# Kernel optimization log

Hardware: AMD Instinct MI355X
Metric: run time of the kernel (lower is better)

The kernel has to match this reference:

```python
import jax, jax.numpy as jnp
import numpy as np

N_A, N_P = 100000, 150000
N = N_A + N_P          # total nodes in concatenated feature matrix
D = 128                # emb_dim == hidden
C = 16                 # num_classes
E = 2000000            # nnz per relation


def setup_inputs() -> dict:
    key = jax.random.key(0)
    ks = jax.random.split(key, 16)
    s = 1.0 / np.sqrt(D)
    # coefficients as in init_coe: uniform(-b, b) then L1-normalized, coe_num = 1+2+2 = 5
    bound = np.sqrt(3.0 / 5)
    coe_np = np.random.RandomState(0).uniform(-bound, bound, 5)
    coe_np = coe_np / np.sum(np.abs(coe_np))
    return {
        "x0": jax.random.normal(ks[0], (N_A, D), jnp.float32),
        "x1": jax.random.normal(ks[1], (N_P, D), jnp.float32),
        "vals_ap": jax.random.uniform(ks[2], (E,), jnp.float32) * 0.01,
        "vals_pa": jax.random.uniform(ks[3], (E,), jnp.float32) * 0.01,
        # AP: rows are A nodes [0, N_A), cols are P nodes [N_A, N)
        "rows_ap": jax.random.randint(ks[4], (E,), 0, N_A, jnp.int32),
        "cols_ap": jax.random.randint(ks[5], (E,), N_A, N, jnp.int32),
        # PA: rows are P nodes [N_A, N), cols are A nodes [0, N_A)
        "rows_pa": jax.random.randint(ks[6], (E,), N_A, N, jnp.int32),
        "cols_pa": jax.random.randint(ks[7], (E,), 0, N_A, jnp.int32),
        "Wp0": jax.random.normal(ks[8], (D, D), jnp.float32) * s,
        "Wp1": jax.random.normal(ks[9], (D, D), jnp.float32) * s,
        "W1": jax.random.normal(ks[10], (D, D), jnp.float32) * s,
        "b1": jnp.zeros((D,), jnp.float32),
        "W2": jax.random.normal(ks[11], (D, C), jnp.float32) * s,
        "b2": jnp.zeros((C,), jnp.float32),
        "coe": jnp.asarray(coe_np, jnp.float32),
    }


def _spmm(rows, cols, vals, h):
    # sparse [N,N] @ dense [N,D] via gather + segment-sum
    return jax.ops.segment_sum(vals[:, None] * h[cols], rows, num_segments=N)


def _normalize(x):
    mean = x.mean(axis=1, keepdims=True)
    std = jnp.std(x, axis=1, keepdims=True, ddof=1)  # torch std is unbiased
    z = (x - mean) / std
    return jnp.where(jnp.isnan(z), 0.0, z)


def _power_pass(x, coe, ap, pa, first_order):
    # first_order: tuple of relation names in hop-1 order ("AP","PA") or ("PA","AP")
    rel = {"AP": ap, "PA": pa}
    res = coe[0] * x
    h = {}
    for ci, r in enumerate(first_order):
        h[r] = _spmm(*rel[r], x)
        res = res + coe[1 + ci] * h[r]
    # hop 2: compose relation j[:2] with previous result j[2:]
    second = [r + first_order[1 - i] for i, r in enumerate(first_order)]
    for ci, j in enumerate(second):
        out = _spmm(*rel[j[:2]], h[j[2:]])
        res = res + coe[3 + ci] * out
    return res


def reference(x0, x1, vals_ap, vals_pa, rows_ap, cols_ap, rows_pa, cols_pa,
              Wp0, Wp1, W1, b1, W2, b2, coe):
    ap = (rows_ap, cols_ap, vals_ap)
    pa = (rows_pa, cols_pa, vals_pa)
    # per-type projection then concat along node axis
    x = jnp.concatenate([x0 @ Wp0, x1 @ Wp1], axis=0)  # [N, D]
    x = jax.nn.relu(x @ W1 + b1)
    x = _normalize(x)
    # pass 1: lis = {1: [AP, PA], 2: [APPA, PAAP]}
    x = _power_pass(x, coe, ap, pa, ("AP", "PA"))
    # pass 2 (transposed series): lis_t = {1: [PA, AP], 2: [PAAP, APPA]}
    res = _power_pass(x, coe, ap, pa, ("PA", "AP"))
    return res @ W2 + b2  # [N, C]
```

## Files before the change

### kernel.cpp

```cpp
#include <hip/hip_runtime.h>
#include <hip/hip_bf16.h>


typedef float f32x2 __attribute__((ext_vector_type(2)));
typedef float f32x4 __attribute__((ext_vector_type(4)));

__device__ inline unsigned short f2bf(float x) {
    unsigned b = __float_as_uint(x);
    unsigned r = (b + 0x7fffu + ((b >> 16) & 1u)) >> 16;
    return (unsigned short)r;
}
__device__ inline float bflo(unsigned u) { return __uint_as_float(u << 16); }
__device__ inline float bfhi(unsigned u) { return __uint_as_float(u & 0xffff0000u); }

__device__ inline unsigned pk_fp8x4(float a, float b, float c, float d) {
    int v = __builtin_amdgcn_cvt_pk_fp8_f32(a, b, 0, false);
    v = __builtin_amdgcn_cvt_pk_fp8_f32(c, d, v, true);
    return (unsigned)v;
}

__global__ __launch_bounds__(128) void fuse_w(const float* __restrict__ Wp0,
                                              const float* __restrict__ Wp1,
                                              const float* __restrict__ W1,
                                              float* __restrict__ M0,
                                              float* __restrict__ M1) {
    int m = blockIdx.x >> 7;
    int i = blockIdx.x & 127;
    const float* Wp = m ? Wp1 : Wp0;
    float* M = m ? M1 : M0;
    __shared__ float r[128];
    int t = threadIdx.x;
    r[t] = Wp[i * 128 + t];
    __syncthreads();
    float acc = 0.f;
    #pragma unroll 8
    for (int k = 0; k < 128; ++k) acc += r[k] * W1[k * 128 + t];
    M[i * 128 + t] = acc;
}

__global__ __launch_bounds__(256) void gemm_relu_norm(const float* __restrict__ xin,
                                                      const float* __restrict__ M,
                                                      const float* __restrict__ b1,
                                                      unsigned short* __restrict__ xbf,
                                                      unsigned char* __restrict__ x8,
                                                      int nrows) {
    __shared__ float Wl[64 * 128];
    __shared__ float xs[32 * 128];
    int t = threadIdx.x;
    long row0 = (long)blockIdx.x * 32;
    int rows_this = nrows - (int)row0;
    if (rows_this > 32) rows_this = 32;

    #pragma unroll
    for (int it = 0; it < 4; ++it) {
        int g4 = it * 256 + t;
        int g = g4 * 4;
        int rl = g >> 7, c = g & 127;
        float4 val = {0.f, 0.f, 0.f, 0.f};
        if (rl < rows_this) val = *(const float4*)(xin + (row0 + rl) * 128 + c);
        *(float4*)&xs[rl * 128 + c] = val;
    }

    int r0 = (t >> 5) * 4;
    int c0 = (t & 31) * 4;
    float acc[4][4];
    #pragma unroll
    for (int i = 0; i < 4; ++i)
        #pragma unroll
        for (int j = 0; j < 4; ++j) acc[i][j] = 0.f;

    for (int h = 0; h < 2; ++h) {
        __syncthreads();
        #pragma unroll
        for (int it = 0; it < 8; ++it) {
            int g4 = it * 256 + t;
            ((float4*)Wl)[g4] = ((const float4*)(M + h * 8192))[g4];
        }
        __syncthreads();
        #pragma unroll 4
        for (int k = 0; k < 64; ++k) {
            float4 w = *(float4*)&Wl[k * 128 + c0];
            int kk = h * 64 + k;
            #pragma unroll
            for (int i = 0; i < 4; ++i) {
                float a = xs[(r0 + i) * 128 + kk];
                acc[i][0] += a * w.x;
                acc[i][1] += a * w.y;
                acc[i][2] += a * w.z;
                acc[i][3] += a * w.w;
            }
        }
    }

    float4 bb = *(const float4*)(b1 + c0);
    #pragma unroll
    for (int i = 0; i < 4; ++i) {
        float o0 = acc[i][0] + bb.x; o0 = o0 > 0.f ? o0 : 0.f;
        float o1 = acc[i][1] + bb.y; o1 = o1 > 0.f ? o1 : 0.f;
        float o2 = acc[i][2] + bb.z; o2 = o2 > 0.f ? o2 : 0.f;
        float o3 = acc[i][3] + bb.w; o3 = o3 > 0.f ? o3 : 0.f;
        float s = o0 + o1 + o2 + o3;
        #pragma unroll
        for (int m = 16; m >= 1; m >>= 1) s += __shfl_xor(s, m);
        float mean = s * (1.0f / 128.0f);
        float d0 = o0 - mean, d1 = o1 - mean, d2 = o2 - mean, d3 = o3 - mean;
        float q = d0 * d0 + d1 * d1 + d2 * d2 + d3 * d3;
        #pragma unroll
        for (int m = 16; m >= 1; m >>= 1) q += __shfl_xor(q, m);
        float inv = 0.f;
        if (q > 0.f) inv = 1.0f / sqrtf(q * (1.0f / 127.0f));
        int row = r0 + i;
        if (row < rows_this) {
            float z0 = d0 * inv, z1 = d1 * inv, z2 = d2 * inv, z3 = d3 * inv;
            uint2 pk;
            pk.x = (unsigned)f2bf(z0) | ((unsigned)f2bf(z1) << 16);
            pk.y = (unsigned)f2bf(z2) | ((unsigned)f2bf(z3) << 16);
            *(uint2*)(xbf + (row0 + row) * 128 + c0) = pk;
            *(unsigned*)(x8 + (row0 + row) * 128 + c0) = pk_fp8x4(z0, z1, z2, z3);
        }
    }
}

__global__ __launch_bounds__(256) void count_rows(const int* __restrict__ rows, int E,
                                                  int* __restrict__ cnt) {
    int i = (blockIdx.x * 256 + threadIdx.x) * 4;
    if (i + 4 <= E) {
        int4 r = *(const int4*)(rows + i);
        atomicAdd(&cnt[r.x], 1);
        atomicAdd(&cnt[r.y], 1);
        atomicAdd(&cnt[r.z], 1);
        atomicAdd(&cnt[r.w], 1);
    } else {
        for (; i < E; ++i) atomicAdd(&cnt[rows[i]], 1);
    }
}

__global__ __launch_bounds__(256) void scan1(const int* __restrict__ cnt, int R,
                                             int* __restrict__ rp, int* __restrict__ bt) {
    __shared__ int lds[256];
    int t = threadIdx.x, b = blockIdx.x;
    int base = b * 4096 + t * 16;
    int v[16];
    int s = 0;
    #pragma unroll
    for (int i = 0; i < 16; ++i) {
        int idx = base + i;
        int c = (idx < R) ? cnt[idx] : 0;
        v[i] = s;
        s += c;
    }
    lds[t] = s;
    __syncthreads();
    for (int off = 1; off < 256; off <<= 1) {
        int x = (t >= off) ? lds[t - off] : 0;
        __syncthreads();
        lds[t] += x;
        __syncthreads();
    }
    int excl = lds[t] - s;
    #pragma unroll
    for (int i = 0; i < 16; ++i) {
        int idx = base + i;
        if (idx < R) rp[idx] = excl + v[i];
    }
    if (t == 0) bt[b] = lds[255];
}

__global__ __launch_bounds__(64) void scan2(const int* __restrict__ bt, int B,
                                            int* __restrict__ bo, int* __restrict__ rp,
                                            int R, int E2) {
    int t = threadIdx.x;
    int v = (t < B) ? bt[t] : 0;
    int inc = v;
    #pragma unroll
    for (int off = 1; off < 64; off <<= 1) {
        int y = __shfl_up(inc, off);
        if (t >= off) inc += y;
    }
    if (t < B) bo[t] = inc - v;
    if (t == 0) rp[R] = E2;
}

__global__ __launch_bounds__(256) void scan3(int* __restrict__ rp, const int* __restrict__ bo,
                                             int R) {
    int i = blockIdx.x * 256 + threadIdx.x;
    if (i < R) rp[i] = rp[i] + bo[i >> 12];
}

__global__ __launch_bounds__(256) void binit(const int* __restrict__ rp, int NR,
                                             int nbuck, int* __restrict__ bcur) {
    int b = blockIdx.x * 256 + threadIdx.x;
    if (b < nbuck) {
        int r = b << 9;
        if (r > NR) r = NR;
        bcur[b] = rp[r];
    }
}

__global__ __launch_bounds__(256) void partition_edges(const int* __restrict__ rows,
                                                       const int* __restrict__ cols,
                                                       const float* __restrict__ vals,
                                                       int E, int nbuck,
                                                       int* __restrict__ bcur,
                                                       int2* __restrict__ tmp) {
    __shared__ int hist[512];
    __shared__ int gbase[512];
    __shared__ int cnt2[512];
    int t = threadIdx.x;
    for (int b = t; b < nbuck; b += 256) { hist[b] = 0; cnt2[b] = 0; }
    __syncthreads();
    long base = (long)blockIdx.x * 4096;
    #pragma unroll
    for (int k = 0; k < 16; ++k) {
        long i = base + k * 256 + t;
        if (i < E) atomicAdd(&hist[rows[i] >> 9], 1);
    }
    __syncthreads();
    for (int b = t; b < nbuck; b += 256) {
        int h = hist[b];
        gbase[b] = h ? atomicAdd(&bcur[b], h) : 0;
    }
    __syncthreads();
    #pragma unroll
    for (int k = 0; k < 16; ++k) {
        long i = base + k * 256 + t;
        if (i < E) {
            int rl = rows[i];
            int b = rl >> 9;
            int rank = atomicAdd(&cnt2[b], 1);
            int2 rec;
            rec.x = ((rl - (b << 9)) << 18) | cols[i];
            rec.y = __float_as_int(vals[i]);
            tmp[gbase[b] + rank] = rec;
        }
    }
}

__global__ __launch_bounds__(1024) void place_edges(const int* __restrict__ rp,
                                                    const int2* __restrict__ tmp,
                                                    int NR,
                                                    int2* __restrict__ scv) {
    __shared__ int hist[512];
    __shared__ int hoff[512];
    int b = blockIdx.x;
    int srow = b << 9;
    int erow = srow + 512;
    if (erow > NR) erow = NR;
    int start = rp[srow], endp = rp[erow];
    int t = threadIdx.x;
    if (t < 512) hist[t] = 0;
    __syncthreads();

    for (int i = start + t; i < endp; i += 1024)
        atomicAdd(&hist[tmp[i].x >> 18], 1);
    __syncthreads();

    if (t < 512) hoff[t] = hist[t];
    __syncthreads();
    for (int off = 1; off < 512; off <<= 1) {
        int v = 0;
        if (t < 512 && t >= off) v = hoff[t - off];
        __syncthreads();
        if (t < 512) hoff[t] += v;
        __syncthreads();
    }
    if (t < 512) hoff[t] = start + hoff[t] - hist[t];
    __syncthreads();

    int i = start + t;
    for (; i + 3 * 1024 < endp; i += 4 * 1024) {
        int2 a0 = tmp[i];
        int2 a1 = tmp[i + 1024];
        int2 a2 = tmp[i + 2048];
        int2 a3 = tmp[i + 3072];
        int p0 = atomicAdd(&hoff[a0.x >> 18], 1);
        int p1 = atomicAdd(&hoff[a1.x >> 18], 1);
        int p2 = atomicAdd(&hoff[a2.x >> 18], 1);
        int p3 = atomicAdd(&hoff[a3.x >> 18], 1);
        int2 o0; o0.x = a0.x & 0x3ffff; o0.y = a0.y;
        int2 o1; o1.x = a1.x & 0x3ffff; o1.y = a1.y;
        int2 o2; o2.x = a2.x & 0x3ffff; o2.y = a2.y;
        int2 o3; o3.x = a3.x & 0x3ffff; o3.y = a3.y;
        scv[p0] = o0;
        scv[p1] = o1;
        scv[p2] = o2;
        scv[p3] = o3;
    }
    for (; i < endp; i += 1024) {
        int2 rec = tmp[i];
        int p = atomicAdd(&hoff[rec.x >> 18], 1);
        int2 o;
        o.x = rec.x & 0x3ffff;
        o.y = rec.y;
        scv[p] = o;
    }
}

#define DEC_FMA(qq, vv) do {                                                        \
    f32x2 vp_ = {(vv), (vv)};                                                       \
    acc[0] = __builtin_elementwise_fma(vp_, __builtin_amdgcn_cvt_pk_f32_fp8((qq).x, false), acc[0]); \
    acc[1] = __builtin_elementwise_fma(vp_, __builtin_amdgcn_cvt_pk_f32_fp8((qq).x, true),  acc[1]); \
    acc[2] = __builtin_elementwise_fma(vp_, __builtin_amdgcn_cvt_pk_f32_fp8((qq).y, false), acc[2]); \
    acc[3] = __builtin_elementwise_fma(vp_, __builtin_amdgcn_cvt_pk_f32_fp8((qq).y, true),  acc[3]); \
} while (0)

__device__ inline void spmm_core8(const int* __restrict__ rp,
                                  const int2* __restrict__ scv,
                                  const unsigned char* __restrict__ g8,
                                  int row, int f, f32x2* acc) {
    int beg = rp[row], end = rp[row + 1];
    int j = beg;
    if ((j & 1) && j < end) {
        int2 r0 = scv[j];
        uint2 q0 = *(const uint2*)(g8 + ((long)r0.x << 7) + f);
        float v0 = __int_as_float(r0.y);
        DEC_FMA(q0, v0);
        ++j;
    }
    for (; j + 8 <= end; j += 8) {
        int4 s01 = *(const int4*)(scv + j);
        int4 s23 = *(const int4*)(scv + j + 2);
        int4 s45 = *(const int4*)(scv + j + 4);
        int4 s67 = *(const int4*)(scv + j + 6);
        uint2 q0 = *(const uint2*)(g8 + ((long)s01.x << 7) + f);
        uint2 q1 = *(const uint2*)(g8 + ((long)s01.z << 7) + f);
        uint2 q2 = *(const uint2*)(g8 + ((long)s23.x << 7) + f);
        uint2 q3 = *(const uint2*)(g8 + ((long)s23.z << 7) + f);
        uint2 q4 = *(const uint2*)(g8 + ((long)s45.x << 7) + f);
        uint2 q5 = *(const uint2*)(g8 + ((long)s45.z << 7) + f);
        uint2 q6 = *(const uint2*)(g8 + ((long)s67.x << 7) + f);
        uint2 q7 = *(const uint2*)(g8 + ((long)s67.z << 7) + f);
        DEC_FMA(q0, __int_as_float(s01.y));
        DEC_FMA(q1, __int_as_float(s01.w));
        DEC_FMA(q2, __int_as_float(s23.y));
        DEC_FMA(q3, __int_as_float(s23.w));
        DEC_FMA(q4, __int_as_float(s45.y));
        DEC_FMA(q5, __int_as_float(s45.w));
        DEC_FMA(q6, __int_as_float(s67.y));
        DEC_FMA(q7, __int_as_float(s67.w));
    }
    for (; j + 2 <= end; j += 2) {
        int4 s01 = *(const int4*)(scv + j);
        uint2 q0 = *(const uint2*)(g8 + ((long)s01.x << 7) + f);
        uint2 q1 = *(const uint2*)(g8 + ((long)s01.z << 7) + f);
        DEC_FMA(q0, __int_as_float(s01.y));
        DEC_FMA(q1, __int_as_float(s01.w));
    }
    if (j < end) {
        int2 r0 = scv[j];
        uint2 q0 = *(const uint2*)(g8 + ((long)r0.x << 7) + f);
        float v0 = __int_as_float(r0.y);
        DEC_FMA(q0, v0);
    }
}

__global__ __launch_bounds__(256) void spmm_plain(const int* __restrict__ rp,
                                                  const int2* __restrict__ scv,
                                                  const unsigned char* __restrict__ x8,
                                                  unsigned short* __restrict__ houtbf,
                                                  unsigned char* __restrict__ hout8,
                                                  int R) {
    int wave = blockIdx.x * 4 + (threadIdx.x >> 6);
    int lane = threadIdx.x & 63;
    int row = wave * 4 + (lane >> 4);
    if (row >= R) return;
    int f = (lane & 15) << 3;
    f32x2 acc[4];
    #pragma unroll
    for (int i = 0; i < 4; ++i) acc[i] = (f32x2){0.f, 0.f};
    spmm_core8(rp, scv, x8, row, f, acc);
    uint4 o;
    o.x = (unsigned)f2bf(acc[0].x) | ((unsigned)f2bf(acc[0].y) << 16);
    o.y = (unsigned)f2bf(acc[1].x) | ((unsigned)f2bf(acc[1].y) << 16);
    o.z = (unsigned)f2bf(acc[2].x) | ((unsigned)f2bf(acc[2].y) << 16);
    o.w = (unsigned)f2bf(acc[3].x) | ((unsigned)f2bf(acc[3].y) << 16);
    *(uint4*)(houtbf + ((long)row << 7) + f) = o;
    uint2 o8;
    o8.x = pk_fp8x4(acc[0].x, acc[0].y, acc[1].x, acc[1].y);
    o8.y = pk_fp8x4(acc[2].x, acc[2].y, acc[3].x, acc[3].y);
    *(uint2*)(hout8 + ((long)row << 7) + f) = o8;
}

__global__ __launch_bounds__(256) void spmm_update(const int* __restrict__ rp,
                                                   const int2* __restrict__ scv,
                                                   const unsigned char* __restrict__ h8,
                                                   const unsigned short* __restrict__ hbf,
                                                   unsigned short* __restrict__ Xbf,
                                                   unsigned char* __restrict__ X8,
                                                   const float* __restrict__ coe,
                                                   int ihA, int iaA, int ihP, int iaP,
                                                   int NA, int R) {
    int wave = blockIdx.x * 4 + (threadIdx.x >> 6);
    int lane = threadIdx.x & 63;
    int row = wave * 4 + (lane >> 4);
    if (row >= R) return;
    int f = (lane & 15) << 3;
    f32x2 acc[4];
    #pragma unroll
    for (int i = 0; i < 4; ++i) acc[i] = (f32x2){0.f, 0.f};
    spmm_core8(rp, scv, h8, row, f, acc);

    float c0 = coe[0];
    float ch = coe[row < NA ? ihA : ihP];
    float ca = coe[row < NA ? iaA : iaP];
    long o = ((long)row << 7) + f;
    uint4 xv = *(const uint4*)(Xbf + o);
    uint4 hs = *(const uint4*)(hbf + o);
    float r[8];
    r[0] = c0 * bflo(xv.x) + ch * bflo(hs.x) + ca * acc[0].x;
    r[1] = c0 * bfhi(xv.x) + ch * bfhi(hs.x) + ca * acc[0].y;
    r[2] = c0 * bflo(xv.y) + ch * bflo(hs.y) + ca * acc[1].x;
    r[3] = c0 * bfhi(xv.y) + ch * bfhi(hs.y) + ca * acc[1].y;
    r[4] = c0 * bflo(xv.z) + ch * bflo(hs.z) + ca * acc[2].x;
    r[5] = c0 * bfhi(xv.z) + ch * bfhi(hs.z) + ca * acc[2].y;
    r[6] = c0 * bflo(xv.w) + ch * bflo(hs.w) + ca * acc[3].x;
    r[7] = c0 * bfhi(xv.w) + ch * bfhi(hs.w) + ca * acc[3].y;
    uint4 ob;
    ob.x = (unsigned)f2bf(r[0]) | ((unsigned)f2bf(r[1]) << 16);
    ob.y = (unsigned)f2bf(r[2]) | ((unsigned)f2bf(r[3]) << 16);
    ob.z = (unsigned)f2bf(r[4]) | ((unsigned)f2bf(r[5]) << 16);
    ob.w = (unsigned)f2bf(r[6]) | ((unsigned)f2bf(r[7]) << 16);
    *(uint4*)(Xbf + o) = ob;
    uint2 o8;
    o8.x = pk_fp8x4(r[0], r[1], r[2], r[3]);
    o8.y = pk_fp8x4(r[4], r[5], r[6], r[7]);
    *(uint2*)(X8 + o) = o8;
}

__global__ __launch_bounds__(256) void spmm_update_out(const int* __restrict__ rp,
                                                       const int2* __restrict__ scv,
                                                       const unsigned char* __restrict__ h8,
                                                       const unsigned short* __restrict__ hbf,
                                                       const unsigned short* __restrict__ Xbf,
                                                       const float* __restrict__ coe,
                                                       const float* __restrict__ W2,
                                                       const float* __restrict__ b2,
                                                       float* __restrict__ out,
                                                       int ihA, int iaA, int ihP, int iaP,
                                                       int NA, int R) {
    __shared__ float xs[16 * 132];
    __shared__ float wT[16 * 132];
    __shared__ float bs[16];
    int t = threadIdx.x;
    #pragma unroll
    for (int i = 0; i < 8; ++i) {
        int idx = i * 256 + t;
        wT[(idx & 15) * 132 + (idx >> 4)] = W2[idx];
    }
    if (t < 16) bs[t] = b2[t];

    int lane = t & 63;
    int rl = (t >> 6) * 4 + (lane >> 4);
    int row = blockIdx.x * 16 + rl;
    int f = (lane & 15) << 3;
    if (row < R) {
        f32x2 acc[4];
        #pragma unroll
        for (int i = 0; i < 4; ++i) acc[i] = (f32x2){0.f, 0.f};
        spmm_core8(rp, scv, h8, row, f, acc);
        float c0 = coe[0];
        float ch = coe[row < NA ? ihA : ihP];
        float ca = coe[row < NA ? iaA : iaP];
        long o = ((long)row << 7) + f;
        uint4 xv = *(const uint4*)(Xbf + o);
        uint4 hs = *(const uint4*)(hbf + o);
        float* x = &xs[rl * 132 + f];
        x[0] = c0 * bflo(xv.x) + ch * bflo(hs.x) + ca * acc[0].x;
        x[1] = c0 * bfhi(xv.x) + ch * bfhi(hs.x) + ca * acc[0].y;
        x[2] = c0 * bflo(xv.y) + ch * bflo(hs.y) + ca * acc[1].x;
        x[3] = c0 * bfhi(xv.y) + ch * bfhi(hs.y) + ca * acc[1].y;
        x[4] = c0 * bflo(xv.z) + ch * bflo(hs.z) + ca * acc[2].x;
        x[5] = c0 * bfhi(xv.z) + ch * bfhi(hs.z) + ca * acc[2].y;
        x[6] = c0 * bflo(xv.w) + ch * bflo(hs.w) + ca * acc[3].x;
        x[7] = c0 * bfhi(xv.w) + ch * bfhi(hs.w) + ca * acc[3].y;
    }
    __syncthreads();
    int orl = t >> 4, c = t & 15;
    long orow = (long)blockIdx.x * 16 + orl;
    if (orow < R) {
        const float* xrow = &xs[orl * 132];
        const float* wrow = &wT[c * 132];
        f32x4 a4 = {0.f, 0.f, 0.f, 0.f};
        #pragma unroll 8
        for (int k = 0; k < 128; k += 4) {
            f32x4 xv = *(const f32x4*)(xrow + k);
            f32x4 wv = *(const f32x4*)(wrow + k);
            a4 = __builtin_elementwise_fma(xv, wv, a4);
        }
        out[orow * 16 + c] = a4.x + a4.y + a4.z + a4.w + bs[c];
    }
}

extern "C" void kernel_launch(void* const* d_in, const int* in_sizes, int n_in,
                              void* d_out, int out_size, void* d_ws, size_t ws_size,
                              hipStream_t stream) {
    const float* x0  = (const float*)d_in[0];
    const float* x1  = (const float*)d_in[1];
    const float* vap = (const float*)d_in[2];
    const float* vpa = (const float*)d_in[3];
    const int*   rap = (const int*)d_in[4];
    const int*   cap = (const int*)d_in[5];
    const int*   rpa = (const int*)d_in[6];
    const int*   cpa = (const int*)d_in[7];
    const float* Wp0 = (const float*)d_in[8];
    const float* Wp1 = (const float*)d_in[9];
    const float* W1  = (const float*)d_in[10];
    const float* b1  = (const float*)d_in[11];
    const float* W2  = (const float*)d_in[12];
    const float* b2  = (const float*)d_in[13];
    const float* coe = (const float*)d_in[14];
    float* out = (float*)d_out;

    const int NA = in_sizes[0] / 128;
    const int NP = in_sizes[1] / 128;
    const int N  = NA + NP;
    const int E  = in_sizes[2];
    const int E2 = 2 * E;

    char* p = (char*)d_ws;
    auto alloc = [&](size_t bytes) {
        char* r = p;
        p += (bytes + 255) & ~(size_t)255;
        return r;
    };
    unsigned short* Xbf = (unsigned short*)alloc((size_t)N * 128 * 2);
    unsigned short* hbf = (unsigned short*)alloc((size_t)N * 128 * 2);
    unsigned char* X8 = (unsigned char*)alloc((size_t)N * 128);
    unsigned char* h8 = (unsigned char*)alloc((size_t)N * 128);
    float* M0  = (float*)alloc(128 * 128 * 4);
    float* M1  = (float*)alloc(128 * 128 * 4);
    int* cnt   = (int*)alloc((size_t)N * 4);
    int* rp    = (int*)alloc((size_t)(N + 1) * 4);
    int* bt    = (int*)alloc(64 * 4);
    int* bo    = (int*)alloc(64 * 4);
    int2* scv  = (int2*)alloc((size_t)E2 * 8);
    int* bcur  = (int*)alloc(512 * 4);
    if ((size_t)(p - (char*)d_ws) > ws_size) return;

    int2* tmp = (int2*)Xbf;

    const int nbuck = (N + 511) >> 9;
    const int pg = (E + 4095) / 4096;

    hipMemsetAsync(cnt, 0, (size_t)N * 4, stream);
    const int cg = (E / 4 + 255) / 256;
    count_rows<<<cg, 256, 0, stream>>>(rap, E, cnt);
    count_rows<<<cg, 256, 0, stream>>>(rpa, E, cnt);
    int B = (N + 4095) / 4096;
    scan1<<<B, 256, 0, stream>>>(cnt, N, rp, bt);
    scan2<<<1, 64, 0, stream>>>(bt, B, bo, rp, N, E2);
    scan3<<<(N + 255) / 256, 256, 0, stream>>>(rp, bo, N);
    binit<<<2, 256, 0, stream>>>(rp, N, nbuck, bcur);
    partition_edges<<<pg, 256, 0, stream>>>(rap, cap, vap, E, nbuck, bcur, tmp);
    partition_edges<<<pg, 256, 0, stream>>>(rpa, cpa, vpa, E, nbuck, bcur, tmp);
    place_edges<<<nbuck, 1024, 0, stream>>>(rp, tmp, N, scv);

    fuse_w<<<256, 128, 0, stream>>>(Wp0, Wp1, W1, M0, M1);
    gemm_relu_norm<<<(NA + 31) / 32, 256, 0, stream>>>(x0, M0, b1, Xbf, X8, NA);
    gemm_relu_norm<<<(NP + 31) / 32, 256, 0, stream>>>(
        x1, M1, b1, Xbf + (size_t)NA * 128, X8 + (size_t)NA * 128, NP);

    const int sg = (N + 15) / 16;

    spmm_plain<<<sg, 256, 0, stream>>>(rp, scv, X8, hbf, h8, N);
    spmm_update<<<sg, 256, 0, stream>>>(rp, scv, h8, hbf, Xbf, X8, coe, 1, 3, 2, 4, NA, N);

    spmm_plain<<<sg, 256, 0, stream>>>(rp, scv, X8, hbf, h8, N);
    spmm_update_out<<<sg, 256, 0, stream>>>(rp, scv, h8, hbf, Xbf, coe,
                                            W2, b2, out, 2, 4, 1, 3, NA, N);
}
```

Baseline: 998.8 us.

## Use bf16 MFMA with hi/lo split for the projection GEMM

```diff
diff --git a/kernel.cpp b/kernel.cpp
--- a/kernel.cpp
+++ b/kernel.cpp
@@ -4,6 +4,7 @@
 
 typedef float f32x2 __attribute__((ext_vector_type(2)));
 typedef float f32x4 __attribute__((ext_vector_type(4)));
+typedef short bf16x8 __attribute__((ext_vector_type(8)));
 
 __device__ inline unsigned short f2bf(float x) {
     unsigned b = __float_as_uint(x);
@@ -22,12 +23,12 @@
 __global__ __launch_bounds__(128) void fuse_w(const float* __restrict__ Wp0,
                                               const float* __restrict__ Wp1,
                                               const float* __restrict__ W1,
-                                              float* __restrict__ M0,
-                                              float* __restrict__ M1) {
+                                              unsigned short* __restrict__ Mt0,
+                                              unsigned short* __restrict__ Mt1) {
     int m = blockIdx.x >> 7;
     int i = blockIdx.x & 127;
     const float* Wp = m ? Wp1 : Wp0;
-    float* M = m ? M1 : M0;
+    unsigned short* Mt = m ? Mt1 : Mt0;
     __shared__ float r[128];
     int t = threadIdx.x;
     r[t] = Wp[i * 128 + t];
@@ -35,88 +36,128 @@
     float acc = 0.f;
     #pragma unroll 8
     for (int k = 0; k < 128; ++k) acc += r[k] * W1[k * 128 + t];
-    M[i * 128 + t] = acc;
+    Mt[t * 128 + i] = f2bf(acc);
 }
 
 __global__ __launch_bounds__(256) void gemm_relu_norm(const float* __restrict__ xin,
-                                                      const float* __restrict__ M,
+                                                      const unsigned short* __restrict__ Mt,
                                                       const float* __restrict__ b1,
                                                       unsigned short* __restrict__ xbf,
                                                       unsigned char* __restrict__ x8,
                                                       int nrows) {
-    __shared__ float Wl[64 * 128];
-    __shared__ float xs[32 * 128];
+    __shared__ char xsh[64 * 256];
+    __shared__ char xsl[64 * 256];
+    __shared__ char mts[128 * 256];
     int t = threadIdx.x;
-    long row0 = (long)blockIdx.x * 32;
+    long row0 = (long)blockIdx.x * 64;
     int rows_this = nrows - (int)row0;
-    if (rows_this > 32) rows_this = 32;
+    if (rows_this > 64) rows_this = 64;
 
     #pragma unroll
     for (int it = 0; it < 4; ++it) {
-        int g4 = it * 256 + t;
-        int g = g4 * 4;
-        int rl = g >> 7, c = g & 127;
-        float4 val = {0.f, 0.f, 0.f, 0.f};
-        if (rl < rows_this) val = *(const float4*)(xin + (row0 + rl) * 128 + c);
-        *(float4*)&xs[rl * 128 + c] = val;
-    }
-
-    int r0 = (t >> 5) * 4;
-    int c0 = (t & 31) * 4;
-    float acc[4][4];
-    #pragma unroll
-    for (int i = 0; i < 4; ++i)
+        int idx = it * 256 + t;
+        int row = idx >> 4, slot = idx & 15;
+        float4 v0 = {0.f, 0.f, 0.f, 0.f}, v1 = {0.f, 0.f, 0.f, 0.f};
+        if (row < rows_this) {
+            v0 = *(const float4*)(xin + (row0 + row) * 128 + slot * 8);
+            v1 = *(const float4*)(xin + (row0 + row) * 128 + slot * 8 + 4);
+        }
+        float vv[8] = {v0.x, v0.y, v0.z, v0.w, v1.x, v1.y, v1.z, v1.w};
+        unsigned hw[8], lw[8];
         #pragma unroll
-        for (int j = 0; j < 4; ++j) acc[i][j] = 0.f;
-
-    for (int h = 0; h < 2; ++h) {
-        __syncthreads();
+        for (int j = 0; j < 8; ++j) {
+            unsigned h = f2bf(vv[j]);
+            float hv = __uint_as_float(h << 16);
+            hw[j] = h;
+            lw[j] = f2bf(vv[j] - hv);
+        }
+        uint4 ph, pl;
+        ph.x = hw[0] | (hw[1] << 16); ph.y = hw[2] | (hw[3] << 16);
+        ph.z = hw[4] | (hw[5] << 16); ph.w = hw[6] | (hw[7] << 16);
+        pl.x = lw[0] | (lw[1] << 16); pl.y = lw[2] | (lw[3] << 16);
+        pl.z = lw[4] | (lw[5] << 16); pl.w = lw[6] | (lw[7] << 16);
+        int off = row * 256 + ((slot ^ (row & 7)) << 4);
+        *(uint4*)&xsh[off] = ph;
+        *(uint4*)&xsl[off] = pl;
+    }
+    #pragma unroll
+    for (int it = 0; it < 8; ++it) {
+        int idx = it * 256 + t;
+        int row = idx >> 4, slot = idx & 15;
+        uint4 mv = ((const uint4*)Mt)[idx];
+        *(uint4*)&mts[row * 256 + ((slot ^ (row & 7)) << 4)] = mv;
+    }
+    __syncthreads();
+
+    int w = t >> 6;
+    int lidx = t & 15;
+    int grp = (t >> 4) & 3;
+    f32x4 acc[8];
+    #pragma unroll
+    for (int nt = 0; nt < 8; ++nt) acc[nt] = (f32x4){0.f, 0.f, 0.f, 0.f};
+
+    #pragma unroll
+    for (int ks = 0; ks < 4; ++ks) {
+        int arow = w * 16 + lidx;
+        int slot = ks * 4 + grp;
+        bf16x8 ah = *(bf16x8*)&xsh[arow * 256 + ((slot ^ (arow & 7)) << 4)];
+        bf16x8 al = *(bf16x8*)&xsl[arow * 256 + ((slot ^ (arow & 7)) << 4)];
         #pragma unroll
-        for (int it = 0; it < 8; ++it) {
-            int g4 = it * 256 + t;
-            ((float4*)Wl)[g4] = ((const float4*)(M + h * 8192))[g4];
-        }
-        __syncthreads();
-        #pragma unroll 4
-        for (int k = 0; k < 64; ++k) {
-            float4 w = *(float4*)&Wl[k * 128 + c0];
-            int kk = h * 64 + k;
-            #pragma unroll
-            for (int i = 0; i < 4; ++i) {
-                float a = xs[(r0 + i) * 128 + kk];
-                acc[i][0] += a * w.x;
-                acc[i][1] += a * w.y;
-                acc[i][2] += a * w.z;
-                acc[i][3] += a * w.w;
-            }
-        }
-    }
-
-    float4 bb = *(const float4*)(b1 + c0);
-    #pragma unroll
-    for (int i = 0; i < 4; ++i) {
-        float o0 = acc[i][0] + bb.x; o0 = o0 > 0.f ? o0 : 0.f;
-        float o1 = acc[i][1] + bb.y; o1 = o1 > 0.f ? o1 : 0.f;
-        float o2 = acc[i][2] + bb.z; o2 = o2 > 0.f ? o2 : 0.f;
-        float o3 = acc[i][3] + bb.w; o3 = o3 > 0.f ? o3 : 0.f;
-        float s = o0 + o1 + o2 + o3;
+        for (int nt = 0; nt < 8; ++nt) {
+            int brow = nt * 16 + lidx;
+            bf16x8 bb = *(bf16x8*)&mts[brow * 256 + ((slot ^ (brow & 7)) << 4)];
+            acc[nt] = __builtin_amdgcn_mfma_f32_16x16x32_bf16(al, bb, acc[nt], 0, 0, 0);
+            acc[nt] = __builtin_amdgcn_mfma_f32_16x16x32_bf16(ah, bb, acc[nt], 0, 0, 0);
+        }
+    }
+
+    float bias[8];
+    #pragma unroll
+    for (int nt = 0; nt < 8; ++nt) bias[nt] = b1[nt * 16 + lidx];
+
+    #pragma unroll
+    for (int r = 0; r < 4; ++r) {
+        int row_loc = w * 16 + grp * 4 + r;
+        float v[8];
+        float s = 0.f;
         #pragma unroll
-        for (int m = 16; m >= 1; m >>= 1) s += __shfl_xor(s, m);
+        for (int nt = 0; nt < 8; ++nt) {
+            float x = acc[nt][r] + bias[nt];
+            x = x > 0.f ? x : 0.f;
+            v[nt] = x;
+            s += x;
+        }
+        s += __shfl_xor(s, 1); s += __shfl_xor(s, 2);
+        s += __shfl_xor(s, 4); s += __shfl_xor(s, 8);
         float mean = s * (1.0f / 128.0f);
-        float d0 = o0 - mean, d1 = o1 - mean, d2 = o2 - mean, d3 = o3 - mean;
-        float q = d0 * d0 + d1 * d1 + d2 * d2 + d3 * d3;
+        float q = 0.f;
         #pragma unroll
-        for (int m = 16; m >= 1; m >>= 1) q += __shfl_xor(q, m);
+        for (int nt = 0; nt < 8; ++nt) {
+            float d = v[nt] - mean;
+            v[nt] = d;
+            q += d * d;
+        }
+        q += __shfl_xor(q, 1); q += __shfl_xor(q, 2);
+        q += __shfl_xor(q, 4); q += __shfl_xor(q, 8);
         float inv = 0.f;
         if (q > 0.f) inv = 1.0f / sqrtf(q * (1.0f / 127.0f));
-        int row = r0 + i;
+        #pragma unroll
+        for (int nt = 0; nt < 8; ++nt)
+            *(unsigned short*)&xsh[row_loc * 256 + (nt * 16 + lidx) * 2] = f2bf(v[nt] * inv);
+    }
+    __syncthreads();
+
+    #pragma unroll
+    for (int it = 0; it < 4; ++it) {
+        int idx = it * 256 + t;
+        int row = idx >> 4, slot = idx & 15;
         if (row < rows_this) {
-            float z0 = d0 * inv, z1 = d1 * inv, z2 = d2 * inv, z3 = d3 * inv;
-            uint2 pk;
-            pk.x = (unsigned)f2bf(z0) | ((unsigned)f2bf(z1) << 16);
-            pk.y = (unsigned)f2bf(z2) | ((unsigned)f2bf(z3) << 16);
-            *(uint2*)(xbf + (row0 + row) * 128 + c0) = pk;
-            *(unsigned*)(x8 + (row0 + row) * 128 + c0) = pk_fp8x4(z0, z1, z2, z3);
+            uint4 zv = *(uint4*)&xsh[row * 256 + slot * 16];
+            *(uint4*)(xbf + (row0 + row) * 128 + slot * 8) = zv;
+            uint2 p8;
+            p8.x = pk_fp8x4(bflo(zv.x), bfhi(zv.x), bflo(zv.y), bfhi(zv.y));
+            p8.y = pk_fp8x4(bflo(zv.z), bfhi(zv.z), bflo(zv.w), bfhi(zv.w));
+            *(uint2*)(x8 + (row0 + row) * 128 + slot * 8) = p8;
         }
     }
 }
@@ -527,8 +568,8 @@
     unsigned short* hbf = (unsigned short*)alloc((size_t)N * 128 * 2);
     unsigned char* X8 = (unsigned char*)alloc((size_t)N * 128);
     unsigned char* h8 = (unsigned char*)alloc((size_t)N * 128);
-    float* M0  = (float*)alloc(128 * 128 * 4);
-    float* M1  = (float*)alloc(128 * 128 * 4);
+    unsigned short* Mt0 = (unsigned short*)alloc(128 * 128 * 2);
+    unsigned short* Mt1 = (unsigned short*)alloc(128 * 128 * 2);
     int* cnt   = (int*)alloc((size_t)N * 4);
     int* rp    = (int*)alloc((size_t)(N + 1) * 4);
     int* bt    = (int*)alloc(64 * 4);
@@ -555,10 +596,10 @@
     partition_edges<<<pg, 256, 0, stream>>>(rpa, cpa, vpa, E, nbuck, bcur, tmp);
     place_edges<<<nbuck, 1024, 0, stream>>>(rp, tmp, N, scv);
 
-    fuse_w<<<256, 128, 0, stream>>>(Wp0, Wp1, W1, M0, M1);
-    gemm_relu_norm<<<(NA + 31) / 32, 256, 0, stream>>>(x0, M0, b1, Xbf, X8, NA);
-    gemm_relu_norm<<<(NP + 31) / 32, 256, 0, stream>>>(
-        x1, M1, b1, Xbf + (size_t)NA * 128, X8 + (size_t)NA * 128, NP);
+    fuse_w<<<256, 128, 0, stream>>>(Wp0, Wp1, W1, Mt0, Mt1);
+    gemm_relu_norm<<<(NA + 63) / 64, 256, 0, stream>>>(x0, Mt0, b1, Xbf, X8, NA);
+    gemm_relu_norm<<<(NP + 63) / 64, 256, 0, stream>>>(
+        x1, Mt1, b1, Xbf + (size_t)NA * 128, X8 + (size_t)NA * 128, NP);
 
     const int sg = (N + 15) / 16;
 
```

Result: faster. 913.4 us (-8.6%).
